# Kernel tuning notes

Hardware: AMD Instinct MI355X
Metric: run time of the kernel (lower is better)

Reference implementation:

```python
import jax, jax.numpy as jnp
import numpy as np

B, N, D = 4096, 200, 64
N_USERS, N_ITEMS, N_RATES = 100000, 100000, 6
EPS = 1e-10


def _linear_params(key, out_dim, in_dim):
    kw, kb = jax.random.split(key)
    bound = 1.0 / np.sqrt(in_dim)
    w = jax.random.uniform(kw, (out_dim, in_dim), jnp.float32, -bound, bound)
    b = jax.random.uniform(kb, (out_dim,), jnp.float32, -bound, bound)
    return w, b


def setup_inputs() -> dict:
    key = jax.random.key(0)
    ks = jax.random.split(key, 12)
    iids = jax.random.randint(ks[0], (B,), 0, N_ITEMS)
    uid_col = jax.random.randint(ks[1], (B, N), 0, N_USERS)  # 0 => padding
    rate_col = jax.random.randint(ks[2], (B, N), 0, N_RATES)
    i_user_pad = jnp.stack([uid_col, rate_col], axis=-1)  # [B, N, 2]
    user_emb = jax.random.normal(ks[3], (N_USERS, D), jnp.float32)
    item_emb = jax.random.normal(ks[4], (N_ITEMS, D), jnp.float32)
    rate_emb = jax.random.normal(ks[5], (N_RATES, D), jnp.float32)
    gu_w1, gu_b1 = _linear_params(ks[6], D, 2 * D)       # g_u layer1: 2D -> D (input_dim//2)
    gu_w2, gu_b2 = _linear_params(ks[7], D, D)           # g_u layer2: D -> D
    att_w1, att_b1 = _linear_params(ks[8], D, 2 * D)     # att layer1: 2D -> D
    att_w2, att_b2 = _linear_params(ks[9], 1, D)         # att layer2: D -> 1
    agg_w, agg_b = _linear_params(ks[10], D, D)          # aggre: D -> D
    return {"iids": iids, "i_user_pad": i_user_pad,
            "user_emb": user_emb, "item_emb": item_emb, "rate_emb": rate_emb,
            "gu_w1": gu_w1, "gu_b1": gu_b1, "gu_w2": gu_w2, "gu_b2": gu_b2,
            "att_w1": att_w1, "att_b1": att_b1, "att_w2": att_w2, "att_b2": att_b2,
            "agg_w": agg_w, "agg_b": agg_b}


def reference(iids, i_user_pad, user_emb, item_emb, rate_emb,
              gu_w1, gu_b1, gu_w2, gu_b2,
              att_w1, att_b1, att_w2, att_b2,
              agg_w, agg_b):
    uid = i_user_pad[:, :, 0]                       # [B, N]
    rid = i_user_pad[:, :, 1]                       # [B, N]
    p_t = user_emb[uid]                             # [B, N, D] neighbor-user gather
    i_user_er = rate_emb[rid]                       # [B, N, D] rating gather
    mask_i = (uid > 0).astype(p_t.dtype)            # [B, N]

    # g_u MLP: Linear(2D->D) + ReLU + Linear(D->D)
    x = jnp.concatenate([p_t, i_user_er], axis=2)   # [B, N, 2D]
    h = jax.nn.relu(jnp.einsum('bnd,kd->bnk', x, gu_w1) + gu_b1)
    f_jt = jnp.einsum('bnd,kd->bnk', h, gu_w2) + gu_b2  # [B, N, D]

    # masked broadcast of target item embedding
    q_j = mask_i[:, :, None] * item_emb[iids][:, None, :]  # [B, N, D]

    # attention MLP: Linear(2D->D) + ReLU + Linear(D->1)
    a = jnp.concatenate([f_jt, q_j], axis=2)        # [B, N, 2D]
    ah = jax.nn.relu(jnp.einsum('bnd,kd->bnk', a, att_w1) + att_b1)
    miu = (jnp.einsum('bnd,kd->bnk', ah, att_w2) + att_b2)[:, :, 0]  # [B, N]

    # exp-softmax over neighbors with masking (faithful to original, no max-subtract)
    miu = jnp.exp(miu) * mask_i
    miu = miu / (jnp.sum(miu, axis=1, keepdims=True) + EPS)

    # weighted sum aggregation + output Linear+ReLU
    agg = jnp.sum(miu[:, :, None] * f_jt, axis=1)   # [B, D]
    z_j = jax.nn.relu(agg @ agg_w.T + agg_b)        # [B, D]
    return z_j
```

## Files before the change

kernel.cpp:

```cpp
#include <hip/hip_runtime.h>
#include <hip/hip_bf16.h>

#define B_SZ 4096
#define N_SZ 200
#define NU_SZ 100000

#define OFF_BFRAG 0
#define OFF_AW1BT 12288
#define OFF_ERC   16384
#define OFF_QC    16768
#define OFF_AGG   278912
#define OFF_SC    541056
#define OFF_H1U   545152
#define WS_NEED_BYTES ((size_t)(OFF_H1U + NU_SZ * 64) * 4)

typedef __attribute__((ext_vector_type(8))) __bf16 bf16x8;
typedef __attribute__((ext_vector_type(4))) __bf16 bf16x4;
typedef __attribute__((ext_vector_type(4))) float f32x4;
typedef __attribute__((ext_vector_type(4))) unsigned u32x4;

__device__ __forceinline__ void split2(float x, unsigned &hi, unsigned &lo) {
    unsigned u = __float_as_uint(x);
    hi = (u + 0x7FFFu + ((u >> 16) & 1u)) >> 16;
    float r = x - __uint_as_float(hi << 16);
    unsigned ul = __float_as_uint(r);
    lo = (ul + 0x7FFFu + ((ul >> 16) & 1u)) >> 16;
}

__global__ void prep1(const float* __restrict__ gu_w1, const float* __restrict__ gu_b1,
                      const float* __restrict__ gu_w2, const float* __restrict__ att_w1,
                      const float* __restrict__ rate_emb, float* __restrict__ ws) {
    const int t0 = blockIdx.x * blockDim.x + threadIdx.x;
    const int stride = blockDim.x * gridDim.x;
    unsigned* wsu = (unsigned*)ws;
    for (int i = t0; i < 12288; i += stride) {
        int frag = i >> 8, within = i & 255, lane = within >> 2, r = within & 3;
        int hl = frag & 1, ct = (frag >> 1) & 3, kt = (frag >> 3) & 1, layer = frag >> 4;
        int col = ct * 16 + (lane & 15);
        int d0 = kt * 32 + 8 * (lane >> 4) + 2 * r;
        float w0, w1v;
        if (layer == 0)      { w0 = gu_w1[col * 128 + d0];  w1v = gu_w1[col * 128 + d0 + 1]; }
        else if (layer == 1) { w0 = gu_w2[col * 64 + d0];   w1v = gu_w2[col * 64 + d0 + 1]; }
        else                 { w0 = att_w1[col * 128 + d0]; w1v = att_w1[col * 128 + d0 + 1]; }
        unsigned h0, l0, h1, l1;
        split2(w0, h0, l0); split2(w1v, h1, l1);
        unsigned lo16 = hl ? l0 : h0;
        unsigned hi16 = hl ? l1 : h1;
        wsu[OFF_BFRAG + i] = lo16 | (hi16 << 16);
    }
    for (int i = t0; i < 4096; i += stride) {
        int d = i >> 6, k = i & 63;
        ws[OFF_AW1BT + i] = att_w1[k * 128 + 64 + d];
    }
    for (int i = t0; i < 384; i += stride) {
        int rr = i >> 6, k = i & 63;
        float a = gu_b1[k];
        for (int d = 0; d < 64; ++d)
            a += gu_w1[k * 128 + 64 + d] * rate_emb[rr * 64 + d];
        ws[OFF_ERC + i] = a;
    }
}

__global__ void prep2_qc(const int* __restrict__ iids, const float* __restrict__ item_emb,
                         const float* __restrict__ ws, float* __restrict__ qc) {
    int b = blockIdx.x, k = threadIdx.x;
    int iid = iids[b];
    const float* awbT = ws + OFF_AW1BT;
    const float* irow = item_emb + (size_t)iid * 64;
    float acc = 0.f;
    for (int d = 0; d < 64; ++d)
        acc = fmaf(awbT[d * 64 + k], irow[d], acc);
    qc[b * 64 + k] = acc;
}

#define LAYER_MFMA(LAYER_ID, ACC, AHARR, BFRAG, LANE)                            \
    _Pragma("unroll")                                                            \
    for (int ct = 0; ct < 4; ++ct) {                                             \
        const unsigned* fb = &BFRAG[((((LAYER_ID) * 2 + 0) * 4 + ct) * 2) * 256 + LANE * 4]; \
        u32x4 bh0 = *(const u32x4*)(fb + 0 * 256);                               \
        u32x4 bh1 = *(const u32x4*)(fb + 8 * 256);                               \
        ACC[ct] = __builtin_amdgcn_mfma_f32_16x16x32_bf16(AHARR[0], __builtin_bit_cast(bf16x8, bh0), ACC[ct], 0, 0, 0); \
        ACC[ct] = __builtin_amdgcn_mfma_f32_16x16x32_bf16(AHARR[1], __builtin_bit_cast(bf16x8, bh1), ACC[ct], 0, 0, 0); \
    }

__global__ __launch_bounds__(64) void prep_h1u(const float* __restrict__ user_emb,
                                               const float* __restrict__ ws,
                                               float* __restrict__ h1u) {
    __shared__ __align__(16) __bf16 XH[16 * 64];
    const int blk = blockIdx.x;
    const int lane = threadIdx.x;
    const int lrow = lane & 15;
    const int lgrp = lane >> 4;
    const int lcol = lane & 15;
    const unsigned* __restrict__ bfrag = (const unsigned*)ws + OFF_BFRAG;

    {
        const int dq = lane & 15;
        const int rowt = lane >> 4;
#pragma unroll
        for (int p = 0; p < 4; ++p) {
            int lr = p * 4 + rowt;
            int u  = blk * 16 + lr;
            float4 v = *(const float4*)(user_emb + (size_t)u * 64 + dq * 4);
            bf16x4 hv = { (__bf16)v.x, (__bf16)v.y, (__bf16)v.z, (__bf16)v.w };
            int g = dq >> 1;
            int idx = lr * 64 + ((g ^ (lr & 7)) << 3) + (dq & 1) * 4;
            *(bf16x4*)&XH[idx] = hv;
        }
    }
    bf16x8 AH[2];
    {
        int s = lrow & 7;
#pragma unroll
        for (int kt = 0; kt < 2; ++kt)
            AH[kt] = *(const bf16x8*)&XH[lrow * 64 + (((kt * 4 + lgrp) ^ s) << 3)];
    }
    f32x4 acc[4];
#pragma unroll
    for (int ct = 0; ct < 4; ++ct)
#pragma unroll
        for (int r = 0; r < 4; ++r) acc[ct][r] = 0.f;
    LAYER_MFMA(0, acc, AH, bfrag, lane)
#pragma unroll
    for (int ct = 0; ct < 4; ++ct)
#pragma unroll
        for (int r = 0; r < 4; ++r)
            h1u[(size_t)(blk * 16 + lgrp * 4 + r) * 64 + ct * 16 + lcol] = acc[ct][r];
}

__global__ __launch_bounds__(64) void fused_main2(
    const int* __restrict__ pad, const float* __restrict__ h1u,
    const float* __restrict__ gu_b2, const float* __restrict__ att_b1,
    const float* __restrict__ att_w2, const float* __restrict__ att_b2,
    const float* __restrict__ ws, float* __restrict__ aggbuf, float* __restrict__ scbuf) {

    __shared__ __align__(16) __bf16 XH[16 * 64];
    __shared__ float erc_s[6 * 65];
    __shared__ float mask_s[16];
    __shared__ float b2_s[64], aw2_s[64], ab1_s[64], qc_s[64];

    const unsigned id = blockIdx.x;
    const int b = id / 13;
    const int t = id - b * 13;
    const int lane = threadIdx.x;
    const int lrow = lane & 15;
    const int lgrp = lane >> 4;
    const int lcol = lane & 15;
    const unsigned* __restrict__ bfrag = (const unsigned*)ws + OFF_BFRAG;
    const float ab2 = att_b2[0];

    b2_s[lane]  = gu_b2[lane];
    aw2_s[lane] = att_w2[lane];
    ab1_s[lane] = att_b1[lane];
    qc_s[lane]  = ws[OFF_QC + b * 64 + lane];
#pragma unroll
    for (int i = 0; i < 6; ++i) {
        int j = i * 64 + lane;
        erc_s[(j >> 6) * 65 + (j & 63)] = ws[OFF_ERC + j];
    }

    {
        const int dq = lane & 15;
        const int rowt = lane >> 4;
#pragma unroll
        for (int p = 0; p < 4; ++p) {
            int lr = p * 4 + rowt;
            int n  = t * 16 + lr;
            int uid = 0, rid = 0;
            float4 v = make_float4(0.f, 0.f, 0.f, 0.f);
            if (n < N_SZ) {
                int2 pr = ((const int2*)pad)[b * N_SZ + n];
                uid = pr.x; rid = pr.y;
                v = *(const float4*)(h1u + (size_t)uid * 64 + dq * 4);
            }
            float h0 = fmaxf(v.x + erc_s[rid * 65 + dq * 4 + 0], 0.f);
            float h1 = fmaxf(v.y + erc_s[rid * 65 + dq * 4 + 1], 0.f);
            float h2 = fmaxf(v.z + erc_s[rid * 65 + dq * 4 + 2], 0.f);
            float h3 = fmaxf(v.w + erc_s[rid * 65 + dq * 4 + 3], 0.f);
            bf16x4 hv = { (__bf16)h0, (__bf16)h1, (__bf16)h2, (__bf16)h3 };
            int g = dq >> 1;
            int idx = lr * 64 + ((g ^ (lr & 7)) << 3) + (dq & 1) * 4;
            *(bf16x4*)&XH[idx] = hv;
            if (dq == 0)
                mask_s[lr] = (n < N_SZ && uid > 0) ? 1.f : 0.f;
        }
    }

    auto loadA = [&](bf16x8 A[2]) {
        int s = lrow & 7;
#pragma unroll
        for (int kt = 0; kt < 2; ++kt)
            A[kt] = *(const bf16x8*)&XH[lrow * 64 + (((kt * 4 + lgrp) ^ s) << 3)];
    };

    f32x4 f_reg[4];
    {
        bf16x8 AH[2];
        loadA(AH);
#pragma unroll
        for (int ct = 0; ct < 4; ++ct) {
            float bb = b2_s[ct * 16 + lcol];
#pragma unroll
            for (int r = 0; r < 4; ++r) f_reg[ct][r] = bb;
        }
        LAYER_MFMA(1, f_reg, AH, bfrag, lane)
#pragma unroll
        for (int ct = 0; ct < 4; ++ct) {
            int col = ct * 16 + lcol;
#pragma unroll
            for (int r = 0; r < 4; ++r) {
                int ln = lgrp * 4 + r;
                int idx = ln * 64 + (((col >> 3) ^ (ln & 7)) << 3) + (col & 7);
                XH[idx] = (__bf16)f_reg[ct][r];
            }
        }
    }

    float aggr[4];
    float swave = 0.f;
    {
        bf16x8 AH[2];
        loadA(AH);
        float maskr[4];
#pragma unroll
        for (int r = 0; r < 4; ++r) maskr[r] = mask_s[lgrp * 4 + r];
        f32x4 acc[4];
#pragma unroll
        for (int ct = 0; ct < 4; ++ct) {
            int k = ct * 16 + lcol;
            float bb = ab1_s[k], qq = qc_s[k];
#pragma unroll
            for (int r = 0; r < 4; ++r) acc[ct][r] = fmaf(maskr[r], qq, bb);
        }
        LAYER_MFMA(2, acc, AH, bfrag, lane)
        float pm[4] = { 0.f, 0.f, 0.f, 0.f };
#pragma unroll
        for (int ct = 0; ct < 4; ++ct) {
            float w2v = aw2_s[ct * 16 + lcol];
#pragma unroll
            for (int r = 0; r < 4; ++r)
                pm[r] = fmaf(fmaxf(acc[ct][r], 0.f), w2v, pm[r]);
        }
#pragma unroll
        for (int off = 1; off <= 8; off <<= 1) {
#pragma unroll
            for (int r = 0; r < 4; ++r) pm[r] += __shfl_xor(pm[r], off);
        }
        float miur[4];
#pragma unroll
        for (int r = 0; r < 4; ++r) {
            miur[r] = __expf(pm[r] + ab2) * maskr[r];
            swave += miur[r];
        }
#pragma unroll
        for (int ct = 0; ct < 4; ++ct) {
            float a = 0.f;
#pragma unroll
            for (int r = 0; r < 4; ++r)
                a = fmaf(miur[r], f_reg[ct][r], a);
            aggr[ct] = a;
        }
    }

#pragma unroll
    for (int ct = 0; ct < 4; ++ct) {
        float v = aggr[ct];
        v += __shfl_xor(v, 16);
        v += __shfl_xor(v, 32);
        aggr[ct] = v;
    }
    swave += __shfl_xor(swave, 16);
    swave += __shfl_xor(swave, 32);
    if (lane < 16) {
#pragma unroll
        for (int ct = 0; ct < 4; ++ct)
            atomicAdd(&aggbuf[b * 64 + ct * 16 + lane], aggr[ct]);
    }
    if (lane == 0)
        atomicAdd(&scbuf[b], swave);
}

__global__ __launch_bounds__(64) void fused_main1(
    const int* __restrict__ pad, const float* __restrict__ user_emb,
    const float* __restrict__ gu_b2, const float* __restrict__ att_b1,
    const float* __restrict__ att_w2, const float* __restrict__ att_b2,
    const float* __restrict__ ws, float* __restrict__ aggbuf, float* __restrict__ scbuf) {

    __shared__ __align__(16) __bf16 XH[16 * 64];
    __shared__ float erc_s[6 * 65];
    __shared__ int   rid_s[16];
    __shared__ float mask_s[16];
    __shared__ float b2_s[64], aw2_s[64], ab1_s[64], qc_s[64];

    const unsigned id = blockIdx.x;
    const int b = id / 13;
    const int t = id - b * 13;
    const int lane = threadIdx.x;
    const int lrow = lane & 15;
    const int lgrp = lane >> 4;
    const int lcol = lane & 15;
    const unsigned* __restrict__ bfrag = (const unsigned*)ws + OFF_BFRAG;
    const float ab2 = att_b2[0];

    b2_s[lane]  = gu_b2[lane];
    aw2_s[lane] = att_w2[lane];
    ab1_s[lane] = att_b1[lane];
    qc_s[lane]  = ws[OFF_QC + b * 64 + lane];
#pragma unroll
    for (int i = 0; i < 6; ++i) {
        int j = i * 64 + lane;
        erc_s[(j >> 6) * 65 + (j & 63)] = ws[OFF_ERC + j];
    }
    {
        const int dq = lane & 15;
        const int rowt = lane >> 4;
#pragma unroll
        for (int p = 0; p < 4; ++p) {
            int lr = p * 4 + rowt;
            int n  = t * 16 + lr;
            int uid = 0, rid = 0;
            float4 v = make_float4(0.f, 0.f, 0.f, 0.f);
            if (n < N_SZ) {
                int2 pr = ((const int2*)pad)[b * N_SZ + n];
                uid = pr.x; rid = pr.y;
                v = *(const float4*)( ( (const float*)user_emb ) + (size_t)uid * 64 + dq * 4);
            }
            bf16x4 hv = { (__bf16)v.x, (__bf16)v.y, (__bf16)v.z, (__bf16)v.w };
            int g = dq >> 1;
            int idx = lr * 64 + ((g ^ (lr & 7)) << 3) + (dq & 1) * 4;
            *(bf16x4*)&XH[idx] = hv;
            if (dq == 0) {
                rid_s[lr]  = (n < N_SZ) ? rid : 0;
                mask_s[lr] = (n < N_SZ && uid > 0) ? 1.f : 0.f;
            }
        }
    }
    auto loadA = [&](bf16x8 A[2]) {
        int s = lrow & 7;
#pragma unroll
        for (int kt = 0; kt < 2; ++kt)
            A[kt] = *(const bf16x8*)&XH[lrow * 64 + (((kt * 4 + lgrp) ^ s) << 3)];
    };
    {
        bf16x8 AH[2];
        loadA(AH);
        int ridr[4];
#pragma unroll
        for (int r = 0; r < 4; ++r) ridr[r] = rid_s[lgrp * 4 + r];
        f32x4 acc[4];
#pragma unroll
        for (int ct = 0; ct < 4; ++ct) {
            int k = ct * 16 + lcol;
#pragma unroll
            for (int r = 0; r < 4; ++r) acc[ct][r] = erc_s[ridr[r] * 65 + k];
        }
        LAYER_MFMA(0, acc, AH, bfrag, lane)
#pragma unroll
        for (int ct = 0; ct < 4; ++ct) {
            int col = ct * 16 + lcol;
#pragma unroll
            for (int r = 0; r < 4; ++r) {
                float hv = fmaxf(acc[ct][r], 0.f);
                int ln = lgrp * 4 + r;
                int idx = ln * 64 + (((col >> 3) ^ (ln & 7)) << 3) + (col & 7);
                XH[idx] = (__bf16)hv;
            }
        }
    }
    f32x4 f_reg[4];
    {
        bf16x8 AH[2];
        loadA(AH);
#pragma unroll
        for (int ct = 0; ct < 4; ++ct) {
            float bb = b2_s[ct * 16 + lcol];
#pragma unroll
            for (int r = 0; r < 4; ++r) f_reg[ct][r] = bb;
        }
        LAYER_MFMA(1, f_reg, AH, bfrag, lane)
#pragma unroll
        for (int ct = 0; ct < 4; ++ct) {
            int col = ct * 16 + lcol;
#pragma unroll
            for (int r = 0; r < 4; ++r) {
                int ln = lgrp * 4 + r;
                int idx = ln * 64 + (((col >> 3) ^ (ln & 7)) << 3) + (col & 7);
                XH[idx] = (__bf16)f_reg[ct][r];
            }
        }
    }
    float aggr[4];
    float swave = 0.f;
    {
        bf16x8 AH[2];
        loadA(AH);
        float maskr[4];
#pragma unroll
        for (int r = 0; r < 4; ++r) maskr[r] = mask_s[lgrp * 4 + r];
        f32x4 acc[4];
#pragma unroll
        for (int ct = 0; ct < 4; ++ct) {
            int k = ct * 16 + lcol;
            float bb = ab1_s[k], qq = qc_s[k];
#pragma unroll
            for (int r = 0; r < 4; ++r) acc[ct][r] = fmaf(maskr[r], qq, bb);
        }
        LAYER_MFMA(2, acc, AH, bfrag, lane)
        float pm[4] = { 0.f, 0.f, 0.f, 0.f };
#pragma unroll
        for (int ct = 0; ct < 4; ++ct) {
            float w2v = aw2_s[ct * 16 + lcol];
#pragma unroll
            for (int r = 0; r < 4; ++r)
                pm[r] = fmaf(fmaxf(acc[ct][r], 0.f), w2v, pm[r]);
        }
#pragma unroll
        for (int off = 1; off <= 8; off <<= 1) {
#pragma unroll
            for (int r = 0; r < 4; ++r) pm[r] += __shfl_xor(pm[r], off);
        }
        float miur[4];
#pragma unroll
        for (int r = 0; r < 4; ++r) {
            miur[r] = __expf(pm[r] + ab2) * maskr[r];
            swave += miur[r];
        }
#pragma unroll
        for (int ct = 0; ct < 4; ++ct) {
            float a = 0.f;
#pragma unroll
            for (int r = 0; r < 4; ++r)
                a = fmaf(miur[r], f_reg[ct][r], a);
            aggr[ct] = a;
        }
    }
#pragma unroll
    for (int ct = 0; ct < 4; ++ct) {
        float v = aggr[ct];
        v += __shfl_xor(v, 16);
        v += __shfl_xor(v, 32);
        aggr[ct] = v;
    }
    swave += __shfl_xor(swave, 16);
    swave += __shfl_xor(swave, 32);
    if (lane < 16) {
#pragma unroll
        for (int ct = 0; ct < 4; ++ct)
            atomicAdd(&aggbuf[b * 64 + ct * 16 + lane], aggr[ct]);
    }
    if (lane == 0)
        atomicAdd(&scbuf[b], swave);
}

__global__ __launch_bounds__(256) void final_z(const float* __restrict__ aggbuf,
                                               const float* __restrict__ scbuf,
                                               const float* __restrict__ agg_w,
                                               const float* __restrict__ agg_b,
                                               float* __restrict__ out) {
    __shared__ float aws[64 * 65];
    int t = threadIdx.x;
    for (int idx = t; idx < 4096; idx += 256)
        aws[(idx >> 6) * 65 + (idx & 63)] = agg_w[idx];
    __syncthreads();
    int g = t >> 6, k = t & 63;
    for (int bi = 0; bi < 2; ++bi) {
        int b = blockIdx.x * 8 + g * 2 + bi;
        const float* arow = aggbuf + b * 64;
        float inv = 1.f / (scbuf[b] + 1e-10f);
        float dot = 0.f;
        for (int d = 0; d < 64; ++d)
            dot = fmaf(aws[k * 65 + d], arow[d], dot);
        out[b * 64 + k] = fmaxf(fmaf(inv, dot, agg_b[k]), 0.f);
    }
}

extern "C" void kernel_launch(void* const* d_in, const int* in_sizes, int n_in,
                              void* d_out, int out_size, void* d_ws, size_t ws_size,
                              hipStream_t stream) {
    const int*   iids     = (const int*)d_in[0];
    const int*   pad      = (const int*)d_in[1];
    const float* user_emb = (const float*)d_in[2];
    const float* item_emb = (const float*)d_in[3];
    const float* rate_emb = (const float*)d_in[4];
    const float* gu_w1    = (const float*)d_in[5];
    const float* gu_b1    = (const float*)d_in[6];
    const float* gu_w2    = (const float*)d_in[7];
    const float* gu_b2    = (const float*)d_in[8];
    const float* att_w1   = (const float*)d_in[9];
    const float* att_b1   = (const float*)d_in[10];
    const float* att_w2   = (const float*)d_in[11];
    const float* att_b2   = (const float*)d_in[12];
    const float* agg_w    = (const float*)d_in[13];
    const float* agg_b    = (const float*)d_in[14];
    float* ws  = (float*)d_ws;
    float* out = (float*)d_out;

    hipLaunchKernelGGL(prep1, dim3(32), dim3(256), 0, stream,
                       gu_w1, gu_b1, gu_w2, att_w1, rate_emb, ws);
    hipLaunchKernelGGL(prep2_qc, dim3(B_SZ), dim3(64), 0, stream,
                       iids, item_emb, ws, ws + OFF_QC);
    hipMemsetAsync(ws + OFF_AGG, 0, (size_t)(B_SZ * 64 + B_SZ) * sizeof(float), stream);

    if (ws_size >= WS_NEED_BYTES) {
        hipLaunchKernelGGL(prep_h1u, dim3(NU_SZ / 16), dim3(64), 0, stream,
                           user_emb, ws, ws + OFF_H1U);
        hipLaunchKernelGGL(fused_main2, dim3(B_SZ * 13), dim3(64), 0, stream,
                           pad, ws + OFF_H1U, gu_b2, att_b1, att_w2, att_b2,
                           ws, ws + OFF_AGG, ws + OFF_SC);
    } else {
        hipLaunchKernelGGL(fused_main1, dim3(B_SZ * 13), dim3(64), 0, stream,
                           pad, user_emb, gu_b2, att_b1, att_w2, att_b2,
                           ws, ws + OFF_AGG, ws + OFF_SC);
    }
    hipLaunchKernelGGL(final_z, dim3(B_SZ / 8), dim3(256), 0, stream,
                       ws + OFF_AGG, ws + OFF_SC, agg_w, agg_b, out);
}
```

Before: 109.0 us.

## Fold gu_w2 into att_w1 and skip the LDS round-trip in the main kernel

Precomputes the product att_w1[:, :64] @ gu_w2 and the matching folded bias in a new prep kernel, so the attention first layer is computed directly from the hidden activations h rather than from f_jt. This removes the bf16 write of f_jt to LDS and its reload. It also builds the MFMA A fragments straight from global h1u loads in registers instead of going through swizzled shared memory. Rounding the composed weight to bf16 changes numerics slightly, and one extra small prep launch is added.

Result: faster. 105.1 us (-3.6%).

```diff
diff --git a/kernel.cpp b/kernel.cpp
--- a/kernel.cpp
+++ b/kernel.cpp
@@ -11,7 +11,9 @@
 #define OFF_QC    16768
 #define OFF_AGG   278912
 #define OFF_SC    541056
-#define OFF_H1U   545152
+#define OFF_W32F  545152
+#define OFF_AB1C  549248
+#define OFF_H1U   549312
 #define WS_NEED_BYTES ((size_t)(OFF_H1U + NU_SZ * 64) * 4)
 
 typedef __attribute__((ext_vector_type(8))) __bf16 bf16x8;
@@ -25,6 +27,12 @@
     float r = x - __uint_as_float(hi << 16);
     unsigned ul = __float_as_uint(r);
     lo = (ul + 0x7FFFu + ((ul >> 16) & 1u)) >> 16;
+}
+
+__device__ __forceinline__ unsigned packbf(float e0, float e1) {
+    __bf16 h0 = (__bf16)e0, h1 = (__bf16)e1;
+    return ((unsigned)__builtin_bit_cast(unsigned short, h1) << 16) |
+           (unsigned)__builtin_bit_cast(unsigned short, h0);
 }
 
 __global__ void prep1(const float* __restrict__ gu_w1, const float* __restrict__ gu_b1,
@@ -61,6 +69,39 @@
     }
 }
 
+__global__ __launch_bounds__(256) void prep_w32(const float* __restrict__ att_w1,
+                                                const float* __restrict__ gu_w2,
+                                                const float* __restrict__ att_b1,
+                                                const float* __restrict__ gu_b2,
+                                                float* __restrict__ ws) {
+    unsigned* w32f = (unsigned*)ws + OFF_W32F;
+    int i = blockIdx.x * 256 + threadIdx.x;
+    {
+        int frag = i >> 8, within = i & 255, lane = within >> 2, r = within & 3;
+        int hl = frag & 1, ct = (frag >> 1) & 3, kt = frag >> 3;
+        int col = ct * 16 + (lane & 15);
+        int d0 = kt * 32 + 8 * (lane >> 4) + 2 * r;
+        if (hl == 0) {
+            float w0 = 0.f, w1v = 0.f;
+            for (int k2 = 0; k2 < 64; ++k2) {
+                float a = att_w1[col * 128 + k2];
+                w0  = fmaf(a, gu_w2[k2 * 64 + d0],     w0);
+                w1v = fmaf(a, gu_w2[k2 * 64 + d0 + 1], w1v);
+            }
+            w32f[i] = packbf(w0, w1v);
+        } else {
+            w32f[i] = 0u;
+        }
+    }
+    if (blockIdx.x == 0 && threadIdx.x < 64) {
+        int k3 = threadIdx.x;
+        float a = att_b1[k3];
+        for (int k2 = 0; k2 < 64; ++k2)
+            a = fmaf(att_w1[k3 * 128 + k2], gu_b2[k2], a);
+        ws[OFF_AB1C + k3] = a;
+    }
+}
+
 __global__ void prep2_qc(const int* __restrict__ iids, const float* __restrict__ item_emb,
                          const float* __restrict__ ws, float* __restrict__ qc) {
     int b = blockIdx.x, k = threadIdx.x;
@@ -93,7 +134,6 @@
     const int lgrp = lane >> 4;
     const int lcol = lane & 15;
     const unsigned* __restrict__ bfrag = (const unsigned*)ws + OFF_BFRAG;
-
     {
         const int dq = lane & 15;
         const int rowt = lane >> 4;
@@ -128,14 +168,146 @@
             h1u[(size_t)(blk * 16 + lgrp * 4 + r) * 64 + ct * 16 + lcol] = acc[ct][r];
 }
 
-__global__ __launch_bounds__(64) void fused_main2(
+__global__ __launch_bounds__(64) void fused_main3(
     const int* __restrict__ pad, const float* __restrict__ h1u,
+    const float* __restrict__ gu_b2, const float* __restrict__ att_w2,
+    const float* __restrict__ att_b2,
+    const float* __restrict__ ws, float* __restrict__ aggbuf, float* __restrict__ scbuf) {
+
+    __shared__ float erc_s[6 * 64];
+    __shared__ float mask_s[16];
+    __shared__ float b2_s[64], aw2_s[64], a1c_s[64], qc_s[64];
+
+    const unsigned id = blockIdx.x;
+    const int b = id / 13;
+    const int t = id - b * 13;
+    const int lane = threadIdx.x;
+    const int lrow = lane & 15;
+    const int lgrp = lane >> 4;
+    const int lcol = lane & 15;
+    const unsigned* __restrict__ bfrag = (const unsigned*)ws + OFF_BFRAG;
+    const unsigned* __restrict__ w32f  = (const unsigned*)ws + OFF_W32F;
+    const float ab2 = att_b2[0];
+
+    b2_s[lane]  = gu_b2[lane];
+    aw2_s[lane] = att_w2[lane];
+    a1c_s[lane] = ws[OFF_AB1C + lane];
+    qc_s[lane]  = ws[OFF_QC + b * 64 + lane];
+#pragma unroll
+    for (int i = 0; i < 6; ++i)
+        erc_s[i * 64 + lane] = ws[OFF_ERC + i * 64 + lane];
+
+    const int n = t * 16 + lrow;
+    const bool valid = (n < N_SZ);
+    int uid = 0, rid = 0;
+    if (valid) {
+        int2 pr = ((const int2*)pad)[b * N_SZ + n];
+        uid = pr.x; rid = pr.y;
+    }
+    if (lane < 16)
+        mask_s[lane] = (valid && uid > 0) ? 1.f : 0.f;
+
+    bf16x8 AH[2];
+#pragma unroll
+    for (int kt = 0; kt < 2; ++kt) {
+        const int ko = kt * 32 + lgrp * 8;
+        float4 a = make_float4(0.f, 0.f, 0.f, 0.f), c = a;
+        if (valid) {
+            const float* hp = h1u + (size_t)uid * 64 + ko;
+            a = *(const float4*)hp;
+            c = *(const float4*)(hp + 4);
+        }
+        float4 ea = *(const float4*)&erc_s[rid * 64 + ko];
+        float4 ec = *(const float4*)&erc_s[rid * 64 + ko + 4];
+        float h0 = fmaxf(a.x + ea.x, 0.f), h1 = fmaxf(a.y + ea.y, 0.f);
+        float h2 = fmaxf(a.z + ea.z, 0.f), h3 = fmaxf(a.w + ea.w, 0.f);
+        float h4 = fmaxf(c.x + ec.x, 0.f), h5 = fmaxf(c.y + ec.y, 0.f);
+        float h6 = fmaxf(c.z + ec.z, 0.f), h7 = fmaxf(c.w + ec.w, 0.f);
+        u32x4 hq = { packbf(h0, h1), packbf(h2, h3), packbf(h4, h5), packbf(h6, h7) };
+        AH[kt] = __builtin_bit_cast(bf16x8, hq);
+    }
+
+    f32x4 f_reg[4];
+#pragma unroll
+    for (int ct = 0; ct < 4; ++ct) {
+        float bb = b2_s[ct * 16 + lcol];
+#pragma unroll
+        for (int r = 0; r < 4; ++r) f_reg[ct][r] = bb;
+    }
+    LAYER_MFMA(1, f_reg, AH, bfrag, lane)
+
+    float maskr[4];
+#pragma unroll
+    for (int r = 0; r < 4; ++r) maskr[r] = mask_s[lgrp * 4 + r];
+    f32x4 acc3[4];
+#pragma unroll
+    for (int ct = 0; ct < 4; ++ct) {
+        int k = ct * 16 + lcol;
+        float bb = a1c_s[k], qq = qc_s[k];
+#pragma unroll
+        for (int r = 0; r < 4; ++r) acc3[ct][r] = fmaf(maskr[r], qq, bb);
+    }
+    LAYER_MFMA(0, acc3, AH, w32f, lane)
+
+    float pm[4] = { 0.f, 0.f, 0.f, 0.f };
+#pragma unroll
+    for (int ct = 0; ct < 4; ++ct) {
+        float w2v = aw2_s[ct * 16 + lcol];
+#pragma unroll
+        for (int r = 0; r < 4; ++r)
+            pm[r] = fmaf(fmaxf(acc3[ct][r], 0.f), w2v, pm[r]);
+    }
+#pragma unroll
+    for (int off = 1; off <= 8; off <<= 1) {
+#pragma unroll
+        for (int r = 0; r < 4; ++r) pm[r] += __shfl_xor(pm[r], off);
+    }
+    float aggr[4];
+    float swave = 0.f;
+    {
+        float miur[4];
+#pragma unroll
+        for (int r = 0; r < 4; ++r) {
+            miur[r] = __expf(pm[r] + ab2) * maskr[r];
+            swave += miur[r];
+        }
+#pragma unroll
+        for (int ct = 0; ct < 4; ++ct) {
+            float a = 0.f;
+#pragma unroll
+            for (int r = 0; r < 4; ++r)
+                a = fmaf(miur[r], f_reg[ct][r], a);
+            aggr[ct] = a;
+        }
+    }
+
+#pragma unroll
+    for (int ct = 0; ct < 4; ++ct) {
+        float v = aggr[ct];
+        v += __shfl_xor(v, 16);
+        v += __shfl_xor(v, 32);
+        aggr[ct] = v;
+    }
+    swave += __shfl_xor(swave, 16);
+    swave += __shfl_xor(swave, 32);
+    if (lane < 16) {
+#pragma unroll
+        for (int ct = 0; ct < 4; ++ct)
+            atomicAdd(&aggbuf[b * 64 + ct * 16 + lane], aggr[ct]);
+    }
+    if (lane == 0)
+        atomicAdd(&scbuf[b], swave);
+}
+
+__global__ __launch_bounds__(64) void fused_main1(
+    const int* __restrict__ pad, const float* __restrict__ user_emb,
     const float* __restrict__ gu_b2, const float* __restrict__ att_b1,
     const float* __restrict__ att_w2, const float* __restrict__ att_b2,
     const float* __restrict__ ws, float* __restrict__ aggbuf, float* __restrict__ scbuf) {
 
     __shared__ __align__(16) __bf16 XH[16 * 64];
     __shared__ float erc_s[6 * 65];
+    __shared__ int   rid_s[16];
     __shared__ float mask_s[16];
     __shared__ float b2_s[64], aw2_s[64], ab1_s[64], qc_s[64];
 
@@ -158,7 +330,6 @@
         int j = i * 64 + lane;
         erc_s[(j >> 6) * 65 + (j & 63)] = ws[OFF_ERC + j];
     }
-
     {
         const int dq = lane & 15;
         const int rowt = lane >> 4;
@@ -171,159 +342,7 @@
             if (n < N_SZ) {
                 int2 pr = ((const int2*)pad)[b * N_SZ + n];
                 uid = pr.x; rid = pr.y;
-                v = *(const float4*)(h1u + (size_t)uid * 64 + dq * 4);
-            }
-            float h0 = fmaxf(v.x + erc_s[rid * 65 + dq * 4 + 0], 0.f);
-            float h1 = fmaxf(v.y + erc_s[rid * 65 + dq * 4 + 1], 0.f);
-            float h2 = fmaxf(v.z + erc_s[rid * 65 + dq * 4 + 2], 0.f);
-            float h3 = fmaxf(v.w + erc_s[rid * 65 + dq * 4 + 3], 0.f);
-            bf16x4 hv = { (__bf16)h0, (__bf16)h1, (__bf16)h2, (__bf16)h3 };
-            int g = dq >> 1;
-            int idx = lr * 64 + ((g ^ (lr & 7)) << 3) + (dq & 1) * 4;
-            *(bf16x4*)&XH[idx] = hv;
-            if (dq == 0)
-                mask_s[lr] = (n < N_SZ && uid > 0) ? 1.f : 0.f;
-        }
-    }
-
-    auto loadA = [&](bf16x8 A[2]) {
-        int s = lrow & 7;
-#pragma unroll
-        for (int kt = 0; kt < 2; ++kt)
-            A[kt] = *(const bf16x8*)&XH[lrow * 64 + (((kt * 4 + lgrp) ^ s) << 3)];
-    };
-
-    f32x4 f_reg[4];
-    {
-        bf16x8 AH[2];
-        loadA(AH);
-#pragma unroll
-        for (int ct = 0; ct < 4; ++ct) {
-            float bb = b2_s[ct * 16 + lcol];
-#pragma unroll
-            for (int r = 0; r < 4; ++r) f_reg[ct][r] = bb;
-        }
-        LAYER_MFMA(1, f_reg, AH, bfrag, lane)
-#pragma unroll
-        for (int ct = 0; ct < 4; ++ct) {
-            int col = ct * 16 + lcol;
-#pragma unroll
-            for (int r = 0; r < 4; ++r) {
-                int ln = lgrp * 4 + r;
-                int idx = ln * 64 + (((col >> 3) ^ (ln & 7)) << 3) + (col & 7);
-                XH[idx] = (__bf16)f_reg[ct][r];
-            }
-        }
-    }
-
-    float aggr[4];
-    float swave = 0.f;
-    {
-        bf16x8 AH[2];
-        loadA(AH);
-        float maskr[4];
-#pragma unroll
-        for (int r = 0; r < 4; ++r) maskr[r] = mask_s[lgrp * 4 + r];
-        f32x4 acc[4];
-#pragma unroll
-        for (int ct = 0; ct < 4; ++ct) {
-            int k = ct * 16 + lcol;
-            float bb = ab1_s[k], qq = qc_s[k];
-#pragma unroll
-            for (int r = 0; r < 4; ++r) acc[ct][r] = fmaf(maskr[r], qq, bb);
-        }
-        LAYER_MFMA(2, acc, AH, bfrag, lane)
-        float pm[4] = { 0.f, 0.f, 0.f, 0.f };
-#pragma unroll
-        for (int ct = 0; ct < 4; ++ct) {
-            float w2v = aw2_s[ct * 16 + lcol];
-#pragma unroll
-            for (int r = 0; r < 4; ++r)
-                pm[r] = fmaf(fmaxf(acc[ct][r], 0.f), w2v, pm[r]);
-        }
-#pragma unroll
-        for (int off = 1; off <= 8; off <<= 1) {
-#pragma unroll
-            for (int r = 0; r < 4; ++r) pm[r] += __shfl_xor(pm[r], off);
-        }
-        float miur[4];
-#pragma unroll
-        for (int r = 0; r < 4; ++r) {
-            miur[r] = __expf(pm[r] + ab2) * maskr[r];
-            swave += miur[r];
-        }
-#pragma unroll
-        for (int ct = 0; ct < 4; ++ct) {
-            float a = 0.f;
-#pragma unroll
-            for (int r = 0; r < 4; ++r)
-                a = fmaf(miur[r], f_reg[ct][r], a);
-            aggr[ct] = a;
-        }
-    }
-
-#pragma unroll
-    for (int ct = 0; ct < 4; ++ct) {
-        float v = aggr[ct];
-        v += __shfl_xor(v, 16);
-        v += __shfl_xor(v, 32);
-        aggr[ct] = v;
-    }
-    swave += __shfl_xor(swave, 16);
-    swave += __shfl_xor(swave, 32);
-    if (lane < 16) {
-#pragma unroll
-        for (int ct = 0; ct < 4; ++ct)
-            atomicAdd(&aggbuf[b * 64 + ct * 16 + lane], aggr[ct]);
-    }
-    if (lane == 0)
-        atomicAdd(&scbuf[b], swave);
-}
-
-__global__ __launch_bounds__(64) void fused_main1(
-    const int* __restrict__ pad, const float* __restrict__ user_emb,
-    const float* __restrict__ gu_b2, const float* __restrict__ att_b1,
-    const float* __restrict__ att_w2, const float* __restrict__ att_b2,
-    const float* __restrict__ ws, float* __restrict__ aggbuf, float* __restrict__ scbuf) {
-
-    __shared__ __align__(16) __bf16 XH[16 * 64];
-    __shared__ float erc_s[6 * 65];
-    __shared__ int   rid_s[16];
-    __shared__ float mask_s[16];
-    __shared__ float b2_s[64], aw2_s[64], ab1_s[64], qc_s[64];
-
-    const unsigned id = blockIdx.x;
-    const int b = id / 13;
-    const int t = id - b * 13;
-    const int lane = threadIdx.x;
-    const int lrow = lane & 15;
-    const int lgrp = lane >> 4;
-    const int lcol = lane & 15;
-    const unsigned* __restrict__ bfrag = (const unsigned*)ws + OFF_BFRAG;
-    const float ab2 = att_b2[0];
-
-    b2_s[lane]  = gu_b2[lane];
-    aw2_s[lane] = att_w2[lane];
-    ab1_s[lane] = att_b1[lane];
-    qc_s[lane]  = ws[OFF_QC + b * 64 + lane];
-#pragma unroll
-    for (int i = 0; i < 6; ++i) {
-        int j = i * 64 + lane;
-        erc_s[(j >> 6) * 65 + (j & 63)] = ws[OFF_ERC + j];
-    }
-    {
-        const int dq = lane & 15;
-        const int rowt = lane >> 4;
-#pragma unroll
-        for (int p = 0; p < 4; ++p) {
-            int lr = p * 4 + rowt;
-            int n  = t * 16 + lr;
-            int uid = 0, rid = 0;
-            float4 v = make_float4(0.f, 0.f, 0.f, 0.f);
-            if (n < N_SZ) {
-                int2 pr = ((const int2*)pad)[b * N_SZ + n];
-                uid = pr.x; rid = pr.y;
-                v = *(const float4*)( ( (const float*)user_emb ) + (size_t)uid * 64 + dq * 4);
+                v = *(const float4*)(user_emb + (size_t)uid * 64 + dq * 4);
             }
             bf16x4 hv = { (__bf16)v.x, (__bf16)v.y, (__bf16)v.z, (__bf16)v.w };
             int g = dq >> 1;
@@ -502,10 +521,12 @@
     hipMemsetAsync(ws + OFF_AGG, 0, (size_t)(B_SZ * 64 + B_SZ) * sizeof(float), stream);
 
     if (ws_size >= WS_NEED_BYTES) {
+        hipLaunchKernelGGL(prep_w32, dim3(16), dim3(256), 0, stream,
+                           att_w1, gu_w2, att_b1, gu_b2, ws);
         hipLaunchKernelGGL(prep_h1u, dim3(NU_SZ / 16), dim3(64), 0, stream,
                            user_emb, ws, ws + OFF_H1U);
-        hipLaunchKernelGGL(fused_main2, dim3(B_SZ * 13), dim3(64), 0, stream,
-                           pad, ws + OFF_H1U, gu_b2, att_b1, att_w2, att_b2,
+        hipLaunchKernelGGL(fused_main3, dim3(B_SZ * 13), dim3(64), 0, stream,
+                           pad, ws + OFF_H1U, gu_b2, att_w2, att_b2,
                            ws, ws + OFF_AGG, ws + OFF_SC);
     } else {
         hipLaunchKernelGGL(fused_main1, dim3(B_SZ * 13), dim3(64), 0, stream,
```
